# Kernel tuning notes

Measured on AMD Instinct MI355X. Metric: run time of the kernel, lower is better.

## Reference

```python
import jax, jax.numpy as jnp
import numpy as np
from jax import lax

H = 16          # num heads
D_CONV = 4      # causal conv kernel width
NORMALIZER = 16.0
EPS = 1e-5


def _causal_conv_silu(x, w):
    # x: [B, L, D], w: [D, W] depthwise causal conv, then silu
    B, L, D = x.shape
    xp = jnp.pad(x, ((0, 0), (D_CONV - 1, 0), (0, 0)))
    y = sum(xp[:, k:k + L, :] * w[:, k] for k in range(D_CONV))
    return jax.nn.silu(y)


def _gla_scan(q, k, v, gk):
    # q,k,gk: [B,H,L,dk]; v: [B,H,L,dv]
    B, h, L, dk = q.shape
    dv = v.shape[-1]
    qT = jnp.moveaxis(q, 2, 0)
    kT = jnp.moveaxis(k, 2, 0)
    vT = jnp.moveaxis(v, 2, 0)
    gT = jnp.moveaxis(gk, 2, 0)

    def step(S, inp):
        qt, kt, vt, gt = inp  # [B,H,dk] / [B,H,dv]
        S = S * jnp.exp(gt)[..., None] + kt[..., None] * vt[..., None, :]
        ot = jnp.einsum('bhk,bhkv->bhv', qt, S)
        return S, ot

    S0 = jnp.zeros((B, h, dk, dv), q.dtype)
    S, o = lax.scan(step, S0, (qT, kT, vT, gT))
    return jnp.moveaxis(o, 0, 2), S  # [B,H,L,dv], final state


def setup_inputs() -> dict:
    key = jax.random.key(0)
    ks = jax.random.split(key, 9)
    L, B, D = 8192, 8, 1024
    s = lambda fan: 1.0 / np.sqrt(fan)
    return {
        'x': jax.random.normal(ks[0], (L, B, D), jnp.float32),
        'conv_w': jax.random.normal(ks[1], (D, D_CONV), jnp.float32) * s(D_CONV),
        'Wq': jax.random.normal(ks[2], (D, D // 2), jnp.float32) * s(D),
        'Wkg': jax.random.normal(ks[3], (D, D // 2), jnp.float32) * s(D),
        'Wv': jax.random.normal(ks[4], (D, D), jnp.float32) * s(D),
        'Wg': jax.random.normal(ks[5], (D, D), jnp.float32) * s(D),
        'bg': jax.random.normal(ks[6], (D,), jnp.float32) * 0.02,
        'Wout': jax.random.normal(ks[7], (D, D), jnp.float32) * s(D),
        'aug_balance': jnp.zeros((D // 2,), jnp.float32),
    }


def reference(x, conv_w, Wq, Wkg, Wv, Wg, bg, Wout, aug_balance):
    # x: [L, B, D] -> [B, L, D]
    xb = jnp.swapaxes(x, 0, 1)
    xb = _causal_conv_silu(xb, conv_w)

    q = xb @ Wq                      # [B,L,D/2]
    k_gate = xb @ Wkg                # [B,L,D/2]
    v = xb @ Wv                      # [B,L,D]
    g = xb @ Wg + bg                 # [B,L,D]

    gk = jax.nn.log_sigmoid(k_gate) / NORMALIZER
    k = 1.0 - jnp.exp(gk)

    B, L, _ = q.shape
    split = lambda t: t.reshape(B, L, H, -1).transpose(0, 2, 1, 3)  # b h l d
    qh, kh, gkh, vh = split(q), split(k), split(gk), split(v)
    dk = qh.shape[-1]

    # fused_chunk_gla default scale = dk ** -0.5 (applied to q internally)
    o, new_state = _gla_scan(qh * (dk ** -0.5), kh, vh, gkh)

    # meta self-augmentation (uses unscaled q)
    aug = aug_balance.reshape(H, dk)
    aug_w = jnp.einsum('bhlk,hk,bhlk->bhl', qh, aug, kh)
    o = o + jax.nn.sigmoid(aug_w[..., None] * vh)

    # group norm: LayerNorm over head_dim, no affine
    mu = o.mean(-1, keepdims=True)
    var = o.var(-1, keepdims=True)
    o = (o - mu) * lax.rsqrt(var + EPS)

    o = o.transpose(0, 2, 1, 3).reshape(B, L, -1)  # [B,L,D]
    out = (jax.nn.silu(g) * o) @ Wout
    return jnp.swapaxes(out, 0, 1), new_state  # [L,B,D], [B,H,dk,dv]
```

## Files before the change

kernel.cpp:

```cpp
#include <hip/hip_runtime.h>
#include <stdint.h>

typedef __attribute__((ext_vector_type(4))) float f32x4;
typedef _Float16 f16x8 __attribute__((ext_vector_type(8)));
typedef __attribute__((ext_vector_type(8))) unsigned short u16x8;
typedef __attribute__((ext_vector_type(2))) unsigned int u32x2;
typedef unsigned short u16;
typedef unsigned int u32;

#define LSEQ 8192
#define BB 8
#define DD 1024
#define MM 65536
#define NCH 128

__device__ __forceinline__ u16 f2h(float f) {
    _Float16 h = (_Float16)f;
    return *(u16*)&h;
}
__device__ __forceinline__ float h2f(u16 u) {
    _Float16 h = *(_Float16*)&u;
    return (float)h;
}

__device__ __forceinline__ void gload_lds16(const void* g, void* l) {
    __builtin_amdgcn_global_load_lds(
        (const __attribute__((address_space(1))) u32*)g,
        (__attribute__((address_space(3))) u32*)l, 16, 0, 0);
}

__global__ __launch_bounds__(256) void k_conv_silu(const float* __restrict__ x,
                                                   const float* __restrict__ w,
                                                   u16* __restrict__ xb) {
    int m = blockIdx.x;
    int b = m >> 13, l = m & 8191;
    int d0 = threadIdx.x * 4;
    f32x4 wv[4];
#pragma unroll
    for (int j = 0; j < 4; j++) wv[j] = *(const f32x4*)&w[(d0 + j) * 4];
    float acc[4] = {0.f, 0.f, 0.f, 0.f};
#pragma unroll
    for (int kk = 0; kk < 4; kk++) {
        int lp = l - 3 + kk;
        if (lp >= 0) {
            f32x4 xv = *(const f32x4*)&x[((size_t)(lp * BB + b)) * DD + d0];
#pragma unroll
            for (int j = 0; j < 4; j++) acc[j] += xv[j] * wv[j][kk];
        }
    }
    u16 o[4];
#pragma unroll
    for (int j = 0; j < 4; j++) {
        float a = acc[j];
        o[j] = f2h(a / (1.f + __expf(-a)));
    }
    u32x2 pk;
    pk.x = (u32)o[0] | ((u32)o[1] << 16);
    pk.y = (u32)o[2] | ((u32)o[3] << 16);
    *(u32x2*)&xb[(size_t)m * DD + d0] = pk;
}

__global__ __launch_bounds__(256) void k_packW(const float* __restrict__ Wq,
                                               const float* __restrict__ Wkg,
                                               const float* __restrict__ Wv,
                                               const float* __restrict__ Wg,
                                               const float* __restrict__ Wout,
                                               u16* __restrict__ Wcat,
                                               u16* __restrict__ WoutT) {
    int idx = blockIdx.x * 256 + threadIdx.x;
    const int T1 = 3072 * 1024;
    if (idx < T1) {
        int n = idx >> 10, kk = idx & 1023;
        float v;
        if (n < 512)        v = Wq [kk * 512 + n];
        else if (n < 1024)  v = Wkg[kk * 512 + (n - 512)];
        else if (n < 2048)  v = Wv [kk * 1024 + (n - 1024)];
        else                v = Wg [kk * 1024 + (n - 2048)];
        Wcat[idx] = f2h(v);
    } else {
        int j = idx - T1;
        if (j < 1024 * 1024) {
            int n = j >> 10, kk = j & 1023;
            WoutT[j] = f2h(Wout[kk * 1024 + n]);
        }
    }
}

template <int MODE>
__device__ __forceinline__ void epi_frag(f32x4 v, int grow0, int gcol,
                                         u16* __restrict__ qo, u16* __restrict__ gko,
                                         u16* __restrict__ ko, u16* __restrict__ vo,
                                         u16* __restrict__ sgo, const float* __restrict__ bg,
                                         float* __restrict__ out) {
#pragma unroll
    for (int rr = 0; rr < 4; rr++) {
        int grow = grow0 + rr;
        float val = v[rr];
        if (MODE == 1) {
            if (gcol < 512) {
                qo[(size_t)grow * 512 + gcol] = f2h(val);
            } else if (gcol < 1024) {
                float ls = fminf(val, 0.f) - log1pf(__expf(-fabsf(val)));
                float gkv = ls * 0.0625f;
                gko[(size_t)grow * 512 + (gcol - 512)] = f2h(gkv);
                ko [(size_t)grow * 512 + (gcol - 512)] = f2h(-expm1f(gkv));
            } else if (gcol < 2048) {
                vo[(size_t)grow * 1024 + (gcol - 1024)] = f2h(val);
            } else {
                float gg = val + bg[gcol - 2048];
                sgo[(size_t)grow * 1024 + (gcol - 2048)] = f2h(gg / (1.f + __expf(-gg)));
            }
        } else {
            int l = grow & 8191, b = grow >> 13;
            out[((size_t)(l * BB + b)) * DD + gcol] = val;
        }
    }
}

template <int MODE>
__global__ __launch_bounds__(256, 2) void k_gemm_bt(
    const u16* __restrict__ A, const u16* __restrict__ Bt, int nt_tiles,
    u16* __restrict__ qo, u16* __restrict__ gko, u16* __restrict__ ko,
    u16* __restrict__ vo, u16* __restrict__ sgo, const float* __restrict__ bg,
    float* __restrict__ out) {
    const int K = 1024;
    __shared__ __align__(16) u16 Sm[28672];
    int tid = threadIdx.x;
    int w = tid >> 6, lane = tid & 63;
    int wm = w >> 1, wn = w & 1;
    int lr = lane & 15, lk = lane >> 4;

    int xcd = blockIdx.x & 7;
    int cidx = blockIdx.x >> 3;
    int grpsz = nt_tiles * 4;
    int grp = cidx / grpsz;
    int r = cidx - grp * grpsz;
    int ntile = r >> 2;
    int mts_per_chunk = (gridDim.x >> 3) / nt_tiles;
    int mtile = xcd * mts_per_chunk + grp * 4 + (r & 3);
    int m0 = mtile << 8, n0 = ntile << 7;

#define DECL_ACC(MT) f32x4 a##MT##_0 = {0.f,0.f,0.f,0.f}, a##MT##_1 = {0.f,0.f,0.f,0.f}, \
                           a##MT##_2 = {0.f,0.f,0.f,0.f}, a##MT##_3 = {0.f,0.f,0.f,0.f};
    DECL_ACC(0) DECL_ACC(1) DECL_ACC(2) DECL_ACC(3)
    DECL_ACC(4) DECL_ACC(5) DECL_ACC(6) DECL_ACC(7)
#undef DECL_ACC

    int gslot = (tid & 3) ^ ((tid >> 3) & 3);
    const u16* gA = A + (size_t)(m0 + (tid >> 2)) * K + gslot * 8;
    const u16* gB = Bt + (size_t)(n0 + (tid >> 2)) * K + gslot * 8;
    char* lA = (char*)Sm + w * 1024;
    char* lB = (char*)Sm + 16384 + w * 1024;

#define STAGE(TT, OB) { \
    int k1 = (TT) << 5; \
    gload_lds16(gA + k1, lA + (OB)); \
    gload_lds16(gA + (size_t)64 * K + k1, lA + (OB) + 4096); \
    gload_lds16(gA + (size_t)128 * K + k1, lA + (OB) + 8192); \
    gload_lds16(gA + (size_t)192 * K + k1, lA + (OB) + 12288); \
    gload_lds16(gB + k1, lB + (OB)); \
    gload_lds16(gB + (size_t)64 * K + k1, lB + (OB) + 4096); }

#define MFMA_ROW(MT) { \
    f16x8 av = *(const f16x8*)&As[(wm * 128 + MT * 16 + lr) * 32 + csl]; \
    a##MT##_0 = __builtin_amdgcn_mfma_f32_16x16x32_f16(av, b0, a##MT##_0, 0, 0, 0); \
    a##MT##_1 = __builtin_amdgcn_mfma_f32_16x16x32_f16(av, b1, a##MT##_1, 0, 0, 0); \
    a##MT##_2 = __builtin_amdgcn_mfma_f32_16x16x32_f16(av, b2, a##MT##_2, 0, 0, 0); \
    a##MT##_3 = __builtin_amdgcn_mfma_f32_16x16x32_f16(av, b3, a##MT##_3, 0, 0, 0); }

#define COMPUTE() { \
    int csl = (lk ^ ((lr >> 1) & 3)) * 8; \
    f16x8 b0 = *(const f16x8*)&Bs[(wn * 64 +  0 + lr) * 32 + csl]; \
    f16x8 b1 = *(const f16x8*)&Bs[(wn * 64 + 16 + lr) * 32 + csl]; \
    f16x8 b2 = *(const f16x8*)&Bs[(wn * 64 + 32 + lr) * 32 + csl]; \
    f16x8 b3 = *(const f16x8*)&Bs[(wn * 64 + 48 + lr) * 32 + csl]; \
    __builtin_amdgcn_s_setprio(1); \
    MFMA_ROW(0) MFMA_ROW(1) MFMA_ROW(2) MFMA_ROW(3) \
    MFMA_ROW(4) MFMA_ROW(5) MFMA_ROW(6) MFMA_ROW(7) \
    __builtin_amdgcn_s_setprio(0); }

    STAGE(0, 0)
    STAGE(1, 24576)

    for (int t = 0; t < 31; ++t) {
        asm volatile("s_waitcnt vmcnt(6)" ::: "memory");
        __builtin_amdgcn_sched_barrier(0);
        __builtin_amdgcn_s_barrier();
        {
            const u16* As = Sm + (t & 1) * 12288;
            const u16* Bs = As + 8192;
            COMPUTE()
        }
        __builtin_amdgcn_s_barrier();
        __builtin_amdgcn_sched_barrier(0);
        if (t < 30) {
            STAGE(t + 2, (t & 1) * 24576)
        }
    }
    asm volatile("s_waitcnt vmcnt(0)" ::: "memory");
    __builtin_amdgcn_sched_barrier(0);
    __builtin_amdgcn_s_barrier();
    {
        const u16* As = Sm + 12288;
        const u16* Bs = As + 8192;
        COMPUTE()
    }
#undef COMPUTE
#undef MFMA_ROW
#undef STAGE

#define EPI_ROW(MT) { \
    int gr0 = m0 + wm * 128 + MT * 16 + lk * 4; \
    epi_frag<MODE>(a##MT##_0, gr0, n0 + wn * 64 +  0 + lr, qo, gko, ko, vo, sgo, bg, out); \
    epi_frag<MODE>(a##MT##_1, gr0, n0 + wn * 64 + 16 + lr, qo, gko, ko, vo, sgo, bg, out); \
    epi_frag<MODE>(a##MT##_2, gr0, n0 + wn * 64 + 32 + lr, qo, gko, ko, vo, sgo, bg, out); \
    epi_frag<MODE>(a##MT##_3, gr0, n0 + wn * 64 + 48 + lr, qo, gko, ko, vo, sgo, bg, out); }
    EPI_ROW(0) EPI_ROW(1) EPI_ROW(2) EPI_ROW(3)
    EPI_ROW(4) EPI_ROW(5) EPI_ROW(6) EPI_ROW(7)
#undef EPI_ROW
}

__global__ __launch_bounds__(64) void k_pass1(const u16* __restrict__ gkb,
                                              const u16* __restrict__ kb,
                                              const u16* __restrict__ vb,
                                              float* __restrict__ Mo,
                                              float* __restrict__ eGC) {
    __shared__ __align__(16) float kkT[64 * 32];
    int bhc = blockIdx.x;
    int c = bhc & 127, bh = bhc >> 7;
    int h = bh & 15, b = bh >> 4;
    int m0 = b * LSEQ + c * 64;
    int lane = threadIdx.x;
    if (lane < 32) {
        int i = lane;
        size_t base = (size_t)m0 * 512 + h * 32 + i;
        float G = 0.f;
        for (int t = 0; t < 64; t++) {
            G += h2f(gkb[base + (size_t)t * 512]);
            G = fmaxf(G, -60.f);
            kkT[t * 32 + i] = h2f(kb[base + (size_t)t * 512]) * __expf(-G);
        }
        eGC[bhc * 32 + i] = __expf(G);
    }
    __syncthreads();
    float Ma[32];
#pragma unroll
    for (int i = 0; i < 32; i++) Ma[i] = 0.f;
    size_t vbase = (size_t)m0 * 1024 + h * 64 + lane;
    for (int t = 0; t < 64; t++) {
        float vj = h2f(vb[vbase + (size_t)t * 1024]);
#pragma unroll
        for (int i4 = 0; i4 < 32; i4 += 4) {
            f32x4 kk4 = *(const f32x4*)&kkT[t * 32 + i4];
            Ma[i4 + 0] += kk4[0] * vj;
            Ma[i4 + 1] += kk4[1] * vj;
            Ma[i4 + 2] += kk4[2] * vj;
            Ma[i4 + 3] += kk4[3] * vj;
        }
    }
    size_t mb = (size_t)bhc * 2048 + lane;
#pragma unroll
    for (int i = 0; i < 32; i++) Mo[mb + i * 64] = Ma[i];
}

__global__ __launch_bounds__(64) void k_pass2(float* Mbuf, float* Sbuf,
                                              const float* __restrict__ eGC,
                                              float* __restrict__ state_out, int aliased) {
    int bh = blockIdx.x;
    int j = threadIdx.x;
    float S[32];
#pragma unroll
    for (int i = 0; i < 32; i++) S[i] = 0.f;
    for (int c = 0; c < NCH; c++) {
        size_t base = ((size_t)bh * NCH + c) * 2048;
        float mv[32], ev[32];
#pragma unroll
        for (int i = 0; i < 32; i++) mv[i] = Mbuf[base + i * 64 + j];
#pragma unroll
        for (int i = 0; i < 32; i++) ev[i] = eGC[(bh * NCH + c) * 32 + i];
        if (aliased) { asm volatile("s_waitcnt vmcnt(0)" ::: "memory"); }
#pragma unroll
        for (int i = 0; i < 32; i++) Sbuf[base + i * 64 + j] = S[i];
#pragma unroll
        for (int i = 0; i < 32; i++) S[i] = (S[i] + mv[i]) * ev[i];
    }
    size_t so = (size_t)bh * 2048 + j;
#pragma unroll
    for (int i = 0; i < 32; i++) state_out[so + i * 64] = S[i];
}

__global__ __launch_bounds__(64) void k_pass3(const u16* __restrict__ qb,
                                              const u16* __restrict__ gkb,
                                              const u16* __restrict__ kb,
                                              const u16* __restrict__ vb,
                                              const u16* __restrict__ sgb,
                                              const float* __restrict__ Sbuf,
                                              const float* __restrict__ aug,
                                              u16* __restrict__ PRE) {
    __shared__ __align__(16) u16 qqT[64 * 32];
    __shared__ __align__(16) u16 kkT[64 * 32];
    __shared__ float awl[64];
    int bhc = blockIdx.x;
    int c = bhc & 127, bh = bhc >> 7;
    int h = bh & 15, b = bh >> 4;
    int m0 = b * LSEQ + c * 64;
    int lane = threadIdx.x;
    const float scale = 0.17677669529663689f;
    if (lane < 32) {
        int i = lane;
        size_t base = (size_t)m0 * 512 + h * 32 + i;
        float G = 0.f;
        for (int t = 0; t < 64; t++) {
            float gkv = h2f(gkb[base + (size_t)t * 512]);
            float qv  = h2f(qb [base + (size_t)t * 512]);
            float kv  = h2f(kb [base + (size_t)t * 512]);
            G += gkv;
            G = fmaxf(G, -60.f);
            qqT[t * 32 + i] = f2h(qv * __expf(G) * scale);
            kkT[t * 32 + i] = f2h(kv * __expf(-G));
        }
    }
    {
        int i = lane & 31;
        int th = (lane >> 5) << 5;
        float augi = aug[h * 32 + i];
        size_t base2 = (size_t)m0 * 512 + h * 32 + i;
        for (int tt = 0; tt < 32; tt++) {
            int t = tt + th;
            float qv = h2f(qb[base2 + (size_t)t * 512]);
            float kv = h2f(kb[base2 + (size_t)t * 512]);
            float p = qv * kv * augi;
            p += __shfl_xor(p, 1);
            p += __shfl_xor(p, 2);
            p += __shfl_xor(p, 4);
            p += __shfl_xor(p, 8);
            p += __shfl_xor(p, 16);
            if (i == 0) awl[t] = p;
        }
    }
    __syncthreads();
    float T[32];
    size_t sb = (size_t)bhc * 2048 + lane;
#pragma unroll
    for (int i = 0; i < 32; i++) T[i] = Sbuf[sb + i * 64];
    size_t vbase = (size_t)m0 * 1024 + h * 64 + lane;
    for (int t = 0; t < 64; t++) {
        float vj  = h2f(vb [vbase + (size_t)t * 1024]);
        float sgj = h2f(sgb[vbase + (size_t)t * 1024]);
        float aw = awl[t];
        float o0 = 0.f, o1 = 0.f, o2 = 0.f, o3 = 0.f;
        u16x8 kk8a = *(const u16x8*)&kkT[t * 32 + 0];
        u16x8 qq8a = *(const u16x8*)&qqT[t * 32 + 0];
        u16x8 kk8b = *(const u16x8*)&kkT[t * 32 + 8];
        u16x8 qq8b = *(const u16x8*)&qqT[t * 32 + 8];
        u16x8 kk8c = *(const u16x8*)&kkT[t * 32 + 16];
        u16x8 qq8c = *(const u16x8*)&qqT[t * 32 + 16];
        u16x8 kk8d = *(const u16x8*)&kkT[t * 32 + 24];
        u16x8 qq8d = *(const u16x8*)&qqT[t * 32 + 24];
#pragma unroll
        for (int e = 0; e < 8; e++) {
            T[e]      += h2f(kk8a[e]) * vj;  o0 += h2f(qq8a[e]) * T[e];
            T[8 + e]  += h2f(kk8b[e]) * vj;  o1 += h2f(qq8b[e]) * T[8 + e];
            T[16 + e] += h2f(kk8c[e]) * vj;  o2 += h2f(qq8c[e]) * T[16 + e];
            T[24 + e] += h2f(kk8d[e]) * vj;  o3 += h2f(qq8d[e]) * T[24 + e];
        }
        float o = (o0 + o1) + (o2 + o3);
        o += 1.f / (1.f + __expf(-aw * vj));
        float s1 = o, s2 = o * o;
#pragma unroll
        for (int msk = 1; msk < 64; msk <<= 1) {
            s1 += __shfl_xor(s1, msk);
            s2 += __shfl_xor(s2, msk);
        }
        float mu = s1 * 0.015625f;
        float var = s2 * 0.015625f - mu * mu;
        float on = (o - mu) * rsqrtf(fmaxf(var, 0.f) + 1e-5f);
        PRE[vbase + (size_t)t * 1024] = f2h(on * sgj);
    }
}

extern "C" void kernel_launch(void* const* d_in, const int* in_sizes, int n_in,
                              void* d_out, int out_size, void* d_ws, size_t ws_size,
                              hipStream_t stream) {
    (void)in_sizes; (void)n_in; (void)out_size;
    const float* x      = (const float*)d_in[0];
    const float* conv_w = (const float*)d_in[1];
    const float* Wq     = (const float*)d_in[2];
    const float* Wkg    = (const float*)d_in[3];
    const float* Wv     = (const float*)d_in[4];
    const float* Wg     = (const float*)d_in[5];
    const float* bg     = (const float*)d_in[6];
    const float* Wout   = (const float*)d_in[7];
    const float* aug    = (const float*)d_in[8];

    char* ws = (char*)d_ws;
    u16*   xb    = (u16*)  (ws + 0);
    u16*   Wcat  = (u16*)  (ws + 134217728);
    u16*   WoutT = (u16*)  (ws + 140509184);
    u16*   qb    = (u16*)  (ws + 142606336);
    u16*   gkb   = (u16*)  (ws + 209715200);
    u16*   kbuf  = (u16*)  (ws + 276824064);
    u16*   sgb   = (u16*)  (ws + 343932928);
    float* Mbuf  = (float*)(ws + 478150656);
    float* eGC   = (float*)(ws + 612368384);
    float* Sb    = (float*)(ws + 614465536);
    const size_t REQ_FULL = 748683264ull;
    int aliased = (ws_size < REQ_FULL) ? 1 : 0;
    float* Sbuf = aliased ? Mbuf : Sb;

    float* out = (float*)d_out;
    float* state_out = out + 67108864;
    u16* vb = (u16*)d_out;

    k_conv_silu<<<dim3(65536), dim3(256), 0, stream>>>(x, conv_w, xb);
    k_packW<<<dim3(16384), dim3(256), 0, stream>>>(Wq, Wkg, Wv, Wg, Wout, Wcat, WoutT);
    k_gemm_bt<1><<<dim3(6144), dim3(256), 0, stream>>>(xb, Wcat, 24,
                                                       qb, gkb, kbuf, vb, sgb, bg, nullptr);
    k_pass1<<<dim3(16384), dim3(64), 0, stream>>>(gkb, kbuf, vb, Mbuf, eGC);
    k_pass2<<<dim3(128), dim3(64), 0, stream>>>(Mbuf, Sbuf, eGC, state_out, aliased);
    k_pass3<<<dim3(16384), dim3(64), 0, stream>>>(qb, gkb, kbuf, vb, sgb, Sbuf, aug, xb );
    k_gemm_bt<2><<<dim3(2048), dim3(256), 0, stream>>>(xb, WoutT, 8,
                                                       nullptr, nullptr, nullptr, nullptr, nullptr, nullptr, out);
}
```

Baseline: 1.821 ms.

## Halve GEMM N-tile for higher occupancy and split pass2 scan across more blocks

Result: faster. 1.706 ms (-6.3%).

```diff
diff --git a/kernel.cpp b/kernel.cpp
--- a/kernel.cpp
+++ b/kernel.cpp
@@ -118,13 +118,13 @@
 }
 
 template <int MODE>
-__global__ __launch_bounds__(256, 2) void k_gemm_bt(
+__global__ __launch_bounds__(256, 3) void k_gemm_bt(
     const u16* __restrict__ A, const u16* __restrict__ Bt, int nt_tiles,
     u16* __restrict__ qo, u16* __restrict__ gko, u16* __restrict__ ko,
     u16* __restrict__ vo, u16* __restrict__ sgo, const float* __restrict__ bg,
     float* __restrict__ out) {
     const int K = 1024;
-    __shared__ __align__(16) u16 Sm[28672];
+    __shared__ __align__(16) u16 Sm[20480];
     int tid = threadIdx.x;
     int w = tid >> 6, lane = tid & 63;
     int wm = w >> 1, wn = w & 1;
@@ -138,17 +138,17 @@
     int ntile = r >> 2;
     int mts_per_chunk = (gridDim.x >> 3) / nt_tiles;
     int mtile = xcd * mts_per_chunk + grp * 4 + (r & 3);
-    int m0 = mtile << 8, n0 = ntile << 7;
-
-#define DECL_ACC(MT) f32x4 a##MT##_0 = {0.f,0.f,0.f,0.f}, a##MT##_1 = {0.f,0.f,0.f,0.f}, \
-                           a##MT##_2 = {0.f,0.f,0.f,0.f}, a##MT##_3 = {0.f,0.f,0.f,0.f};
+    int m0 = mtile << 8, n0 = ntile << 6;
+
+#define DECL_ACC(MT) f32x4 a##MT##_0 = {0.f,0.f,0.f,0.f}, a##MT##_1 = {0.f,0.f,0.f,0.f};
     DECL_ACC(0) DECL_ACC(1) DECL_ACC(2) DECL_ACC(3)
     DECL_ACC(4) DECL_ACC(5) DECL_ACC(6) DECL_ACC(7)
 #undef DECL_ACC
 
-    int gslot = (tid & 3) ^ ((tid >> 3) & 3);
-    const u16* gA = A + (size_t)(m0 + (tid >> 2)) * K + gslot * 8;
-    const u16* gB = Bt + (size_t)(n0 + (tid >> 2)) * K + gslot * 8;
+    int row = tid >> 2;
+    int sslot = (tid & 3) ^ (row & 3);
+    const u16* gA = A + (size_t)(m0 + row) * K + sslot * 8;
+    const u16* gB = Bt + (size_t)(n0 + row) * K + sslot * 8;
     char* lA = (char*)Sm + w * 1024;
     char* lB = (char*)Sm + 16384 + w * 1024;
 
@@ -158,50 +158,45 @@
     gload_lds16(gA + (size_t)64 * K + k1, lA + (OB) + 4096); \
     gload_lds16(gA + (size_t)128 * K + k1, lA + (OB) + 8192); \
     gload_lds16(gA + (size_t)192 * K + k1, lA + (OB) + 12288); \
-    gload_lds16(gB + k1, lB + (OB)); \
-    gload_lds16(gB + (size_t)64 * K + k1, lB + (OB) + 4096); }
+    gload_lds16(gB + k1, lB + (OB)); }
 
 #define MFMA_ROW(MT) { \
-    f16x8 av = *(const f16x8*)&As[(wm * 128 + MT * 16 + lr) * 32 + csl]; \
+    f16x8 av = *(const f16x8*)&As[(wm * 128 + MT * 16 + lr) * 32 + acsl]; \
     a##MT##_0 = __builtin_amdgcn_mfma_f32_16x16x32_f16(av, b0, a##MT##_0, 0, 0, 0); \
-    a##MT##_1 = __builtin_amdgcn_mfma_f32_16x16x32_f16(av, b1, a##MT##_1, 0, 0, 0); \
-    a##MT##_2 = __builtin_amdgcn_mfma_f32_16x16x32_f16(av, b2, a##MT##_2, 0, 0, 0); \
-    a##MT##_3 = __builtin_amdgcn_mfma_f32_16x16x32_f16(av, b3, a##MT##_3, 0, 0, 0); }
+    a##MT##_1 = __builtin_amdgcn_mfma_f32_16x16x32_f16(av, b1, a##MT##_1, 0, 0, 0); }
 
 #define COMPUTE() { \
-    int csl = (lk ^ ((lr >> 1) & 3)) * 8; \
-    f16x8 b0 = *(const f16x8*)&Bs[(wn * 64 +  0 + lr) * 32 + csl]; \
-    f16x8 b1 = *(const f16x8*)&Bs[(wn * 64 + 16 + lr) * 32 + csl]; \
-    f16x8 b2 = *(const f16x8*)&Bs[(wn * 64 + 32 + lr) * 32 + csl]; \
-    f16x8 b3 = *(const f16x8*)&Bs[(wn * 64 + 48 + lr) * 32 + csl]; \
+    int acsl = (lk ^ (lr & 3)) * 8; \
+    f16x8 b0 = *(const f16x8*)&Bs[(wn * 32 +  0 + lr) * 32 + acsl]; \
+    f16x8 b1 = *(const f16x8*)&Bs[(wn * 32 + 16 + lr) * 32 + acsl]; \
     __builtin_amdgcn_s_setprio(1); \
     MFMA_ROW(0) MFMA_ROW(1) MFMA_ROW(2) MFMA_ROW(3) \
     MFMA_ROW(4) MFMA_ROW(5) MFMA_ROW(6) MFMA_ROW(7) \
     __builtin_amdgcn_s_setprio(0); }
 
     STAGE(0, 0)
-    STAGE(1, 24576)
+    STAGE(1, 20480)
 
     for (int t = 0; t < 31; ++t) {
-        asm volatile("s_waitcnt vmcnt(6)" ::: "memory");
+        asm volatile("s_waitcnt vmcnt(5)" ::: "memory");
         __builtin_amdgcn_sched_barrier(0);
         __builtin_amdgcn_s_barrier();
         {
-            const u16* As = Sm + (t & 1) * 12288;
+            const u16* As = Sm + (t & 1) * 10240;
             const u16* Bs = As + 8192;
             COMPUTE()
         }
         __builtin_amdgcn_s_barrier();
         __builtin_amdgcn_sched_barrier(0);
         if (t < 30) {
-            STAGE(t + 2, (t & 1) * 24576)
+            STAGE(t + 2, (t & 1) * 20480)
         }
     }
     asm volatile("s_waitcnt vmcnt(0)" ::: "memory");
     __builtin_amdgcn_sched_barrier(0);
     __builtin_amdgcn_s_barrier();
     {
-        const u16* As = Sm + 12288;
+        const u16* As = Sm + 10240;
         const u16* Bs = As + 8192;
         COMPUTE()
     }
@@ -211,10 +206,8 @@
 
 #define EPI_ROW(MT) { \
     int gr0 = m0 + wm * 128 + MT * 16 + lk * 4; \
-    epi_frag<MODE>(a##MT##_0, gr0, n0 + wn * 64 +  0 + lr, qo, gko, ko, vo, sgo, bg, out); \
-    epi_frag<MODE>(a##MT##_1, gr0, n0 + wn * 64 + 16 + lr, qo, gko, ko, vo, sgo, bg, out); \
-    epi_frag<MODE>(a##MT##_2, gr0, n0 + wn * 64 + 32 + lr, qo, gko, ko, vo, sgo, bg, out); \
-    epi_frag<MODE>(a##MT##_3, gr0, n0 + wn * 64 + 48 + lr, qo, gko, ko, vo, sgo, bg, out); }
+    epi_frag<MODE>(a##MT##_0, gr0, n0 + wn * 32 +  0 + lr, qo, gko, ko, vo, sgo, bg, out); \
+    epi_frag<MODE>(a##MT##_1, gr0, n0 + wn * 32 + 16 + lr, qo, gko, ko, vo, sgo, bg, out); }
     EPI_ROW(0) EPI_ROW(1) EPI_ROW(2) EPI_ROW(3)
     EPI_ROW(4) EPI_ROW(5) EPI_ROW(6) EPI_ROW(7)
 #undef EPI_ROW
@@ -266,27 +259,29 @@
 __global__ __launch_bounds__(64) void k_pass2(float* Mbuf, float* Sbuf,
                                               const float* __restrict__ eGC,
                                               float* __restrict__ state_out, int aliased) {
-    int bh = blockIdx.x;
+    int blk = blockIdx.x;
+    int bh = blk >> 2, iq = blk & 3;
+    int i0 = iq * 8;
     int j = threadIdx.x;
-    float S[32];
-#pragma unroll
-    for (int i = 0; i < 32; i++) S[i] = 0.f;
+    float S[8];
+#pragma unroll
+    for (int i = 0; i < 8; i++) S[i] = 0.f;
     for (int c = 0; c < NCH; c++) {
         size_t base = ((size_t)bh * NCH + c) * 2048;
-        float mv[32], ev[32];
-#pragma unroll
-        for (int i = 0; i < 32; i++) mv[i] = Mbuf[base + i * 64 + j];
-#pragma unroll
-        for (int i = 0; i < 32; i++) ev[i] = eGC[(bh * NCH + c) * 32 + i];
+        float mv[8], ev[8];
+#pragma unroll
+        for (int i = 0; i < 8; i++) mv[i] = Mbuf[base + (i0 + i) * 64 + j];
+#pragma unroll
+        for (int i = 0; i < 8; i++) ev[i] = eGC[(bh * NCH + c) * 32 + i0 + i];
         if (aliased) { asm volatile("s_waitcnt vmcnt(0)" ::: "memory"); }
 #pragma unroll
-        for (int i = 0; i < 32; i++) Sbuf[base + i * 64 + j] = S[i];
-#pragma unroll
-        for (int i = 0; i < 32; i++) S[i] = (S[i] + mv[i]) * ev[i];
+        for (int i = 0; i < 8; i++) Sbuf[base + (i0 + i) * 64 + j] = S[i];
+#pragma unroll
+        for (int i = 0; i < 8; i++) S[i] = (S[i] + mv[i]) * ev[i];
     }
     size_t so = (size_t)bh * 2048 + j;
 #pragma unroll
-    for (int i = 0; i < 32; i++) state_out[so + i * 64] = S[i];
+    for (int i = 0; i < 8; i++) state_out[so + (i0 + i) * 64] = S[i];
 }
 
 __global__ __launch_bounds__(64) void k_pass3(const u16* __restrict__ qb,
@@ -414,11 +409,11 @@
 
     k_conv_silu<<<dim3(65536), dim3(256), 0, stream>>>(x, conv_w, xb);
     k_packW<<<dim3(16384), dim3(256), 0, stream>>>(Wq, Wkg, Wv, Wg, Wout, Wcat, WoutT);
-    k_gemm_bt<1><<<dim3(6144), dim3(256), 0, stream>>>(xb, Wcat, 24,
-                                                       qb, gkb, kbuf, vb, sgb, bg, nullptr);
+    k_gemm_bt<1><<<dim3(12288), dim3(256), 0, stream>>>(xb, Wcat, 48,
+                                                        qb, gkb, kbuf, vb, sgb, bg, nullptr);
     k_pass1<<<dim3(16384), dim3(64), 0, stream>>>(gkb, kbuf, vb, Mbuf, eGC);
-    k_pass2<<<dim3(128), dim3(64), 0, stream>>>(Mbuf, Sbuf, eGC, state_out, aliased);
+    k_pass2<<<dim3(512), dim3(64), 0, stream>>>(Mbuf, Sbuf, eGC, state_out, aliased);
     k_pass3<<<dim3(16384), dim3(64), 0, stream>>>(qb, gkb, kbuf, vb, sgb, Sbuf, aug, xb );
-    k_gemm_bt<2><<<dim3(2048), dim3(256), 0, stream>>>(xb, WoutT, 8,
+    k_gemm_bt<2><<<dim3(4096), dim3(256), 0, stream>>>(xb, WoutT, 16,
                                                        nullptr, nullptr, nullptr, nullptr, nullptr, nullptr, out);
 }
```
